# Kernel optimization log

Hardware: AMD Instinct MI355X
Metric: run time of the kernel (lower is better)

The kernel has to match this reference:

```python
import jax, jax.numpy as jnp
import numpy as np

ALLPASS_DELAYS = [225, 556, 441, 341]
ALLPASS_G = 0.7
COMB_DELAYS = [1116, 1188, 1277, 1356]
COMB_FEEDBACKS = [0.84, 0.82, 0.80, 0.78]


def _lagged_first_order(x, N, g, allpass):
    """Fixed-lag first-order recurrence along axis 0, vectorized over axis 1.

    allpass: y[n] = -g*y[n-N] + x[n] + g*x[n-N]  (n >= N), y[n<N] = 0
    comb:    y[n] =  g*y[n-N] + x[n]             (n >= N), y[n<N] = 0

    The recurrence decouples into N independent stride-N subsequences, so we
    reshape to [blocks, N, W] and lax.scan over blocks (T/N steps instead of T).
    """
    T, W = x.shape
    blocks = -(-T // N)
    Tp = blocks * N
    xb = jnp.pad(x, ((0, Tp - T), (0, 0))).reshape(blocks, N, W)
    zero_blk = jnp.zeros((1, N, W), x.dtype)
    if allpass:
        # drive u[k] = x[k] + g*x[k-1]; block 0 output is forced to zero
        u = jnp.concatenate([zero_blk, xb[1:] + g * xb[:-1]], axis=0)
        a = -g
    else:
        # comb: drive u[k] = x[k] for k>=1; block 0 output is zero
        u = jnp.concatenate([zero_blk, xb[1:]], axis=0)
        a = g

    def step(prev, uk):
        y = uk + a * prev
        return y, y

    _, yb = jax.lax.scan(step, jnp.zeros((N, W), x.dtype), u)
    return yb.reshape(Tp, W)[:T]


def setup_inputs() -> dict:
    key = jax.random.key(0)
    T, W = 131072, 128
    x = jax.random.normal(key, (T, W), dtype=jnp.float32)
    return {"x": x}


def reference(x):
    # Series allpass chain
    for N in ALLPASS_DELAYS:
        x = _lagged_first_order(x, N, ALLPASS_G, allpass=True)
    # Parallel feedback comb bank, summed
    comb = jnp.zeros_like(x)
    for N, g in zip(COMB_DELAYS, COMB_FEEDBACKS):
        comb = comb + _lagged_first_order(x, N, g, allpass=False)
    # Original applies eye(T) @ comb and slices [:, :W]; both are identity ops,
    # so we return comb directly (same math, without materializing a TxT eye).
    return comb
```

## Files before the change

kernel.cpp:

```cpp
#include <hip/hip_runtime.h>


constexpr int W = 128;

template <int V> struct fv { float d[V]; };

template <int V>
__device__ __forceinline__ fv<V> fv_zero() {
  fv<V> r;
#pragma unroll
  for (int c = 0; c < V; ++c) r.d[c] = 0.f;
  return r;
}
using fv2 = fv<2>;
using fv4 = fv<4>;

template <int K, bool PRED, int V>
__device__ __forceinline__
void fmarch_blk(const fv<V>* __restrict__ sb, int n0, int N, int laneoff,
                int Tn, float a, fv<V>& yp, fv<V>* __restrict__ y) {
  constexpr int RW = W / V;
  fv<V> xs[K];
#pragma unroll
  for (int u = 0; u < K; ++u) {
    const int n = n0 + u * N;
    xs[u] = (!PRED || n < Tn) ? sb[n * RW + laneoff] : fv_zero<V>();
  }
#pragma unroll
  for (int u = 0; u < K; ++u) {
#pragma unroll
    for (int c = 0; c < V; ++c)
      yp.d[c] = fmaf(a, yp.d[c], xs[u].d[c]);
    y[u] = yp;
  }
}

template <int CNT, bool PRED, int V, int U>
__device__ __forceinline__
void fmarch_seg(const fv<V>* __restrict__ sb, int n0, int N, int laneoff,
                int Tn, float a, fv<V>& yp, fv<V>* __restrict__ y) {
  constexpr int NB = CNT / U, R = CNT % U;
#pragma unroll
  for (int b = 0; b < NB; ++b)
    fmarch_blk<U, PRED, V>(sb, n0 + b * U * N, N, laneoff, Tn, a, yp, y + b * U);
  if constexpr (R > 0)
    fmarch_blk<R, PRED, V>(sb, n0 + NB * U * N, N, laneoff, Tn, a, yp,
                           y + NB * U);
}

template <int MODE, int K, bool PRED, int V>
__device__ __forceinline__
void fstore_blk(fv<V>* __restrict__ out, int n0, int N, int laneoff, int Tn,
                float a, fv<V> Yin, const fv<V>* __restrict__ y, float& p) {
  constexpr int RW = W / V;
  fv<V> os[K];
  if constexpr (MODE == 2) {
#pragma unroll
    for (int u = 0; u < K; ++u) {
      const int n = n0 + u * N;
      os[u] = (!PRED || n < Tn) ? out[n * RW + laneoff] : fv_zero<V>();
    }
  }
#pragma unroll
  for (int u = 0; u < K; ++u) {
    const int n = n0 + u * N;
    fv<V> v;
#pragma unroll
    for (int c = 0; c < V; ++c) {
      v.d[c] = fmaf(p, Yin.d[c], y[u].d[c]);
      if constexpr (MODE == 2) v.d[c] += os[u].d[c];
    }
    if (!PRED || n < Tn) out[n * RW + laneoff] = v;
    p *= a;
  }
}

template <int MODE, int CNT, bool PRED, int V, int U>
__device__ __forceinline__
void fstore_seg(fv<V>* __restrict__ out, int n0, int N, int laneoff, int Tn,
                float a, fv<V> Yin, const fv<V>* __restrict__ y, float p0) {
  constexpr int NB = CNT / U, R = CNT % U;
  float p = p0;
#pragma unroll
  for (int b = 0; b < NB; ++b)
    fstore_blk<MODE, U, PRED, V>(out, n0 + b * U * N, N, laneoff, Tn, a, Yin,
                                 y + b * U, p);
  if constexpr (R > 0)
    fstore_blk<MODE, R, PRED, V>(out, n0 + NB * U * N, N, laneoff, Tn, a, Yin,
                                 y + NB * U, p);
}

template <int MODE, int S, int L, int UM, int US>
__global__ __launch_bounds__(S * 64, 3)
void fcomb(const fv2* __restrict__ sb, fv2* __restrict__ out,
           int N, float g, float aL, int T, int items) {
  const float a = g;
  __shared__ fv2 C[S][64];
  const int tid = threadIdx.x;
  const int s  = tid >> 6;
  const int l6 = tid & 63;

  for (int item = blockIdx.x; item < items; item += gridDim.x) {
    const int r  = item;
    const int n0 = s * L * N + r;

    fv2 y[L];
    fv2 yp = fv_zero<2>();

    if (s == 0) {
      y[0] = fv_zero<2>();
      fmarch_seg<L - 1, false, 2, UM>(sb, n0 + N, N, l6, T, a, yp, y + 1);
    } else if (s < S - 1) {
      fmarch_seg<L, false, 2, UM>(sb, n0, N, l6, T, a, yp, y);
    } else {
      fmarch_seg<L, true, 2, UM>(sb, n0, N, l6, T, a, yp, y);
    }
    C[s][l6] = yp;
    __syncthreads();

    fv2 Yin = fv_zero<2>();
    for (int j = 0; j < s; ++j) {
#pragma unroll
      for (int c = 0; c < 2; ++c)
        Yin.d[c] = fmaf(aL, Yin.d[c], C[j][l6].d[c]);
    }
    __syncthreads();

    if (s < S - 1)
      fstore_seg<MODE, L, false, 2, US>(out, n0, N, l6, T, a, Yin, y, a);
    else
      fstore_seg<MODE, L, true, 2, US>(out, n0, N, l6, T, a, Yin, y, a);
  }
}

__global__ __launch_bounds__(1024)
void prep_s(const fv4* __restrict__ x, fv4* __restrict__ sb) {
  const int e = blockIdx.x * 1024 + threadIdx.x;
  const int n  = e >> 5;
  const int lo = e & 31;
  const int q1 = n / 225, r1 = n - q1 * 225;
  const int q2 = n / 556, r2 = n - q2 * 556;
  const float LG = -0.5145731728297583f;
  const float m1 = exp2f((float)q1 * LG);
  const float m2 = exp2f((float)q2 * LG);
  const float p1 = (q1 & 1) ? -m1 : m1;
  const float p2 = (q2 & 1) ? -m2 : m2;

  const fv4 xs = x[e];
  const fv4 t1 = x[r1 * 32 + lo];
  fv4 t2;
  if (r2 < 225) {
    t2 = fv_zero<4>();
  } else {
    t2 = x[r2 * 32 + lo];
    const int   d = (r2 < 450) ? 225 : 450;
    const float c = (r2 < 450) ? 0.7f : -0.49f;
    const fv4 tt = x[(r2 - d) * 32 + lo];
#pragma unroll
    for (int k = 0; k < 4; ++k) t2.d[k] = fmaf(c, tt.d[k], t2.d[k]);
  }
  fv4 v;
#pragma unroll
  for (int k = 0; k < 4; ++k) {
    float sv = fmaf(-p1, t1.d[k], xs.d[k]);
    v.d[k] = fmaf(-p2, t2.d[k], sv);
  }
  sb[e] = v;
}

constexpr int W2 = 64;
template <int MODE, bool STORE>
__device__ __forceinline__
void g_march(const float2* __restrict__ in, float2* __restrict__ out,
             int n, int N, int cnt, int T, int lane, float g, float a,
             float2& xp, float2& yp) {
  for (int j = 0; j < cnt; ++j) {
    float2 x = (n < T) ? in[n * W2 + lane] : make_float2(0.f, 0.f);
    float ux = (MODE == 0) ? fmaf(g, xp.x, x.x) : x.x;
    float uy = (MODE == 0) ? fmaf(g, xp.y, x.y) : x.y;
    yp.x = fmaf(a, yp.x, ux);
    yp.y = fmaf(a, yp.y, uy);
    xp = x;
    if (STORE && n < T) {
      float2 v = yp;
      if (MODE == 2) { v.x += out[n * W2 + lane].x; v.y += out[n * W2 + lane].y; }
      out[n * W2 + lane] = v;
    }
    n += N;
  }
}

template <int MODE>
__global__ __launch_bounds__(1024)
void stage_gen(const float2* __restrict__ in, float2* __restrict__ out,
               int N, float g, float aL, int L, int T) {
  const float a = (MODE == 0) ? -g : g;
  __shared__ float2 C[16][W2];
  const int tid = threadIdx.x, s = tid >> 6, lane = tid & 63;
  const int r = blockIdx.x;
  if (r >= T) return;
  const int n0 = s * L * N + r;
  if (s == 0) {
    float2 xp = make_float2(0.f, 0.f), yp = make_float2(0.f, 0.f);
    if (MODE == 0) xp = in[r * W2 + lane];
    if (MODE != 2) out[r * W2 + lane] = make_float2(0.f, 0.f);
    g_march<MODE, true>(in, out, r + N, N, L - 1, T, lane, g, a, xp, yp);
    C[0][lane] = yp;
    __syncthreads();
    return;
  }
  {
    float2 xp = make_float2(0.f, 0.f), yp = make_float2(0.f, 0.f);
    if (MODE == 0) xp = in[(n0 - N) * W2 + lane];
    g_march<MODE, false>(in, out, n0, N, L, T, lane, g, a, xp, yp);
    C[s][lane] = yp;
  }
  __syncthreads();
  float2 Yin = make_float2(0.f, 0.f);
  for (int j = 0; j < s; ++j) {
    Yin.x = fmaf(aL, Yin.x, C[j][lane].x);
    Yin.y = fmaf(aL, Yin.y, C[j][lane].y);
  }
  float2 xp = make_float2(0.f, 0.f), yp = Yin;
  if (MODE == 0) xp = in[(n0 - N) * W2 + lane];
  g_march<MODE, true>(in, out, n0, N, L, T, lane, g, a, xp, yp);
}

static void pick_SL(int T, int N, int S0, int* Sp, int* Lp) {
  int Kmin = T / N, Kmax = (T + N - 1) / N;
  int S = S0;
  for (; S > 1; --S) {
    int L = (Kmax + S - 1) / S;
    if ((S - 1) * L <= Kmin) break;
  }
  *Sp = S;
  *Lp = (Kmax + *Sp - 1) / *Sp;
}

static float pow_f(float a, int n) {
  double p = 1.0;
  for (int i = 0; i < n; ++i) p *= (double)a;
  return (float)p;
}

extern "C" void kernel_launch(void* const* d_in, const int* in_sizes, int n_in,
                              void* d_out, int out_size, void* d_ws, size_t ws_size,
                              hipStream_t stream) {
  float* out = (float*)d_out;
  float* ws  = (float*)d_ws;
  const float* x = (const float*)d_in[0];
  const int T = in_sizes[0] / W;

  if (T == 131072) {
    float* sbf = ws;

    hipLaunchKernelGGL(prep_s, dim3(4096), dim3(1024), 0, stream,
                       (const fv4*)x, (fv4*)sbf);

    const fv2* s2 = (const fv2*)sbf;
    fv2* o2 = (fv2*)out;

    hipLaunchKernelGGL((fcomb<1, 8, 15, 4, 4>), dim3(1024), dim3(512),
                       0, stream, s2, o2, 1116, 0.84f, pow_f(0.84f, 15), T, 1116);
    hipLaunchKernelGGL((fcomb<2, 8, 14, 4, 4>), dim3(1024), dim3(512),
                       0, stream, s2, o2, 1188, 0.82f, pow_f(0.82f, 14), T, 1188);
    hipLaunchKernelGGL((fcomb<2, 8, 13, 4, 4>), dim3(1024), dim3(512),
                       0, stream, s2, o2, 1277, 0.80f, pow_f(0.80f, 13), T, 1277);
    hipLaunchKernelGGL((fcomb<2, 8, 13, 4, 4>), dim3(1024), dim3(512),
                       0, stream, s2, o2, 1356, 0.78f, pow_f(0.78f, 13), T, 1356);
  } else {
    const int   apN[4] = {225, 556, 441, 341};
    const int   cbN[4] = {1116, 1188, 1277, 1356};
    const float cbG[4] = {0.84f, 0.82f, 0.80f, 0.78f};
    const float2* src = (const float2*)x;
    float2* bufs[2] = {(float2*)out, (float2*)ws};
    int cur = 0;
    for (int i = 0; i < 4; ++i) {
      int S, L;
      pick_SL(T, apN[i], 16, &S, &L);
      hipLaunchKernelGGL((stage_gen<0>), dim3(apN[i]), dim3(S * 64), 0, stream,
                         src, bufs[cur], apN[i], 0.7f, pow_f(-0.7f, L), L, T);
      src = bufs[cur];
      cur ^= 1;
    }
    float2* dst = (src == (float2*)out) ? (float2*)ws : (float2*)out;
    for (int i = 0; i < 4; ++i) {
      int S, L;
      pick_SL(T, cbN[i], 16, &S, &L);
      if (i == 0)
        hipLaunchKernelGGL((stage_gen<1>), dim3(cbN[i]), dim3(S * 64), 0, stream,
                           src, dst, cbN[i], cbG[i], pow_f(cbG[i], L), L, T);
      else
        hipLaunchKernelGGL((stage_gen<2>), dim3(cbN[i]), dim3(S * 64), 0, stream,
                           src, dst, cbN[i], cbG[i], pow_f(cbG[i], L), L, T);
    }
    if (dst != (float2*)out)
      hipMemcpyAsync(out, dst, (size_t)T * W * sizeof(float),
                     hipMemcpyDeviceToDevice, stream);
  }
}
```

Measured before the change: 227.0 us.

## Fuse allpass prep into first comb pass and store intermediate in fp16

Removes the separate prep_s kernel and computes the allpass-transformed signal inside the first comb kernel, which also writes it out as half precision. The remaining three comb kernels read the fp16 intermediate, halving their input traffic, and unroll their march loads more deeply. The aim is to save one full read-write pass and reduce memory bandwidth. In exchange, precision drops from fp32 to fp16 on the intermediate, which may hurt accuracy. The first kernel also does heavier per-element work, including the gathers at r1 and r2, with lower occupancy (launch bound 2).

```diff
diff --git a/kernel.cpp b/kernel.cpp
--- a/kernel.cpp
+++ b/kernel.cpp
@@ -15,92 +15,157 @@
 using fv2 = fv<2>;
 using fv4 = fv<4>;
 
-template <int K, bool PRED, int V>
-__device__ __forceinline__
-void fmarch_blk(const fv<V>* __restrict__ sb, int n0, int N, int laneoff,
-                int Tn, float a, fv<V>& yp, fv<V>* __restrict__ y) {
-  constexpr int RW = W / V;
-  fv<V> xs[K];
+struct h2 { _Float16 d[2]; };
+
+template <int K, bool PRED>
+__device__ __forceinline__
+void hmarch_blk(const h2* __restrict__ sb, int n0, int N, int lane,
+                int Tn, float a, fv2& yp, fv2* __restrict__ y) {
+  h2 xs[K];
 #pragma unroll
   for (int u = 0; u < K; ++u) {
     const int n = n0 + u * N;
-    xs[u] = (!PRED || n < Tn) ? sb[n * RW + laneoff] : fv_zero<V>();
-  }
-#pragma unroll
-  for (int u = 0; u < K; ++u) {
-#pragma unroll
-    for (int c = 0; c < V; ++c)
-      yp.d[c] = fmaf(a, yp.d[c], xs[u].d[c]);
+    if (!PRED || n < Tn) {
+      xs[u] = sb[n * 64 + lane];
+    } else {
+      xs[u].d[0] = (_Float16)0.f;
+      xs[u].d[1] = (_Float16)0.f;
+    }
+  }
+#pragma unroll
+  for (int u = 0; u < K; ++u) {
+    yp.d[0] = fmaf(a, yp.d[0], (float)xs[u].d[0]);
+    yp.d[1] = fmaf(a, yp.d[1], (float)xs[u].d[1]);
     y[u] = yp;
   }
 }
 
-template <int CNT, bool PRED, int V, int U>
-__device__ __forceinline__
-void fmarch_seg(const fv<V>* __restrict__ sb, int n0, int N, int laneoff,
-                int Tn, float a, fv<V>& yp, fv<V>* __restrict__ y) {
+template <int CNT, bool PRED, int U>
+__device__ __forceinline__
+void hmarch_seg(const h2* __restrict__ sb, int n0, int N, int lane,
+                int Tn, float a, fv2& yp, fv2* __restrict__ y) {
   constexpr int NB = CNT / U, R = CNT % U;
 #pragma unroll
   for (int b = 0; b < NB; ++b)
-    fmarch_blk<U, PRED, V>(sb, n0 + b * U * N, N, laneoff, Tn, a, yp, y + b * U);
+    hmarch_blk<U, PRED>(sb, n0 + b * U * N, N, lane, Tn, a, yp, y + b * U);
   if constexpr (R > 0)
-    fmarch_blk<R, PRED, V>(sb, n0 + NB * U * N, N, laneoff, Tn, a, yp,
-                           y + NB * U);
-}
-
-template <int MODE, int K, bool PRED, int V>
-__device__ __forceinline__
-void fstore_blk(fv<V>* __restrict__ out, int n0, int N, int laneoff, int Tn,
-                float a, fv<V> Yin, const fv<V>* __restrict__ y, float& p) {
-  constexpr int RW = W / V;
-  fv<V> os[K];
+    hmarch_blk<R, PRED>(sb, n0 + NB * U * N, N, lane, Tn, a, yp, y + NB * U);
+}
+
+template <int K, bool PRED>
+__device__ __forceinline__
+void cmarch_blk(const fv2* __restrict__ x, h2* __restrict__ sb,
+                int n0, int N, int lane, int Tn, float a,
+                fv2& yp, fv2* __restrict__ y) {
+  fv2 xs[K], t1[K], t2[K];
+  float p1[K], p2[K];
+#pragma unroll
+  for (int u = 0; u < K; ++u) {
+    const int n = n0 + u * N;
+    const bool ok = !PRED || n < Tn;
+    const int q1 = n / 225, r1 = n - q1 * 225;
+    const int q2 = n / 556, r2 = n - q2 * 556;
+    xs[u] = ok ? x[n * 64 + lane] : fv_zero<2>();
+    t1[u] = x[r1 * 64 + lane];
+    if (r2 < 225) {
+      t2[u] = fv_zero<2>();
+    } else {
+      fv2 b = x[r2 * 64 + lane];
+      const int   d = (r2 < 450) ? 225 : 450;
+      const float c = (r2 < 450) ? 0.7f : -0.49f;
+      fv2 tt = x[(r2 - d) * 64 + lane];
+      t2[u].d[0] = fmaf(c, tt.d[0], b.d[0]);
+      t2[u].d[1] = fmaf(c, tt.d[1], b.d[1]);
+    }
+    const float LG = -0.5145731728297583f;
+    const float m1 = exp2f((float)q1 * LG);
+    const float m2 = exp2f((float)q2 * LG);
+    p1[u] = ok ? ((q1 & 1) ? -m1 : m1) : 0.f;
+    p2[u] = ok ? ((q2 & 1) ? -m2 : m2) : 0.f;
+  }
+#pragma unroll
+  for (int u = 0; u < K; ++u) {
+    const int n = n0 + u * N;
+    fv2 s;
+    s.d[0] = fmaf(-p2[u], t2[u].d[0], fmaf(-p1[u], t1[u].d[0], xs[u].d[0]));
+    s.d[1] = fmaf(-p2[u], t2[u].d[1], fmaf(-p1[u], t1[u].d[1], xs[u].d[1]));
+    if (!PRED || n < Tn) {
+      h2 hh;
+      hh.d[0] = (_Float16)s.d[0];
+      hh.d[1] = (_Float16)s.d[1];
+      sb[n * 64 + lane] = hh;
+    }
+    yp.d[0] = fmaf(a, yp.d[0], s.d[0]);
+    yp.d[1] = fmaf(a, yp.d[1], s.d[1]);
+    y[u] = yp;
+  }
+}
+
+template <int CNT, bool PRED, int U>
+__device__ __forceinline__
+void cmarch_seg(const fv2* __restrict__ x, h2* __restrict__ sb,
+                int n0, int N, int lane, int Tn, float a,
+                fv2& yp, fv2* __restrict__ y) {
+  constexpr int NB = CNT / U, R = CNT % U;
+#pragma unroll
+  for (int b = 0; b < NB; ++b)
+    cmarch_blk<U, PRED>(x, sb, n0 + b * U * N, N, lane, Tn, a, yp, y + b * U);
+  if constexpr (R > 0)
+    cmarch_blk<R, PRED>(x, sb, n0 + NB * U * N, N, lane, Tn, a, yp, y + NB * U);
+}
+
+template <int MODE, int K, bool PRED>
+__device__ __forceinline__
+void fstore_blk(fv2* __restrict__ out, int n0, int N, int lane, int Tn,
+                float a, fv2 Yin, const fv2* __restrict__ y, float& p) {
+  fv2 os[K];
   if constexpr (MODE == 2) {
 #pragma unroll
     for (int u = 0; u < K; ++u) {
       const int n = n0 + u * N;
-      os[u] = (!PRED || n < Tn) ? out[n * RW + laneoff] : fv_zero<V>();
+      os[u] = (!PRED || n < Tn) ? out[n * 64 + lane] : fv_zero<2>();
     }
   }
 #pragma unroll
   for (int u = 0; u < K; ++u) {
     const int n = n0 + u * N;
-    fv<V> v;
-#pragma unroll
-    for (int c = 0; c < V; ++c) {
+    fv2 v;
+#pragma unroll
+    for (int c = 0; c < 2; ++c) {
       v.d[c] = fmaf(p, Yin.d[c], y[u].d[c]);
       if constexpr (MODE == 2) v.d[c] += os[u].d[c];
     }
-    if (!PRED || n < Tn) out[n * RW + laneoff] = v;
+    if (!PRED || n < Tn) out[n * 64 + lane] = v;
     p *= a;
   }
 }
 
-template <int MODE, int CNT, bool PRED, int V, int U>
-__device__ __forceinline__
-void fstore_seg(fv<V>* __restrict__ out, int n0, int N, int laneoff, int Tn,
-                float a, fv<V> Yin, const fv<V>* __restrict__ y, float p0) {
+template <int MODE, int CNT, bool PRED, int U>
+__device__ __forceinline__
+void fstore_seg(fv2* __restrict__ out, int n0, int N, int lane, int Tn,
+                float a, fv2 Yin, const fv2* __restrict__ y, float p0) {
   constexpr int NB = CNT / U, R = CNT % U;
   float p = p0;
 #pragma unroll
   for (int b = 0; b < NB; ++b)
-    fstore_blk<MODE, U, PRED, V>(out, n0 + b * U * N, N, laneoff, Tn, a, Yin,
-                                 y + b * U, p);
+    fstore_blk<MODE, U, PRED>(out, n0 + b * U * N, N, lane, Tn, a, Yin,
+                              y + b * U, p);
   if constexpr (R > 0)
-    fstore_blk<MODE, R, PRED, V>(out, n0 + NB * U * N, N, laneoff, Tn, a, Yin,
-                                 y + NB * U, p);
-}
-
-template <int MODE, int S, int L, int UM, int US>
-__global__ __launch_bounds__(S * 64, 3)
-void fcomb(const fv2* __restrict__ sb, fv2* __restrict__ out,
-           int N, float g, float aL, int T, int items) {
+    fstore_blk<MODE, R, PRED>(out, n0 + NB * U * N, N, lane, Tn, a, Yin,
+                              y + NB * U, p);
+}
+
+template <int S, int L, int UM, int US>
+__global__ __launch_bounds__(S * 64, 2)
+void fcomb1(const fv2* __restrict__ x, h2* __restrict__ sb,
+            fv2* __restrict__ out, int N, float g, float aL, int T) {
   const float a = g;
   __shared__ fv2 C[S][64];
   const int tid = threadIdx.x;
   const int s  = tid >> 6;
   const int l6 = tid & 63;
 
-  for (int item = blockIdx.x; item < items; item += gridDim.x) {
+  for (int item = blockIdx.x; item < N; item += gridDim.x) {
     const int r  = item;
     const int n0 = s * L * N + r;
 
@@ -109,11 +174,11 @@
 
     if (s == 0) {
       y[0] = fv_zero<2>();
-      fmarch_seg<L - 1, false, 2, UM>(sb, n0 + N, N, l6, T, a, yp, y + 1);
+      cmarch_seg<L - 1, false, UM>(x, sb, n0 + N, N, l6, T, a, yp, y + 1);
     } else if (s < S - 1) {
-      fmarch_seg<L, false, 2, UM>(sb, n0, N, l6, T, a, yp, y);
+      cmarch_seg<L, false, UM>(x, sb, n0, N, l6, T, a, yp, y);
     } else {
-      fmarch_seg<L, true, 2, UM>(sb, n0, N, l6, T, a, yp, y);
+      cmarch_seg<L, true, UM>(x, sb, n0, N, l6, T, a, yp, y);
     }
     C[s][l6] = yp;
     __syncthreads();
@@ -127,45 +192,53 @@
     __syncthreads();
 
     if (s < S - 1)
-      fstore_seg<MODE, L, false, 2, US>(out, n0, N, l6, T, a, Yin, y, a);
+      fstore_seg<1, L, false, US>(out, n0, N, l6, T, a, Yin, y, a);
     else
-      fstore_seg<MODE, L, true, 2, US>(out, n0, N, l6, T, a, Yin, y, a);
-  }
-}
-
-__global__ __launch_bounds__(1024)
-void prep_s(const fv4* __restrict__ x, fv4* __restrict__ sb) {
-  const int e = blockIdx.x * 1024 + threadIdx.x;
-  const int n  = e >> 5;
-  const int lo = e & 31;
-  const int q1 = n / 225, r1 = n - q1 * 225;
-  const int q2 = n / 556, r2 = n - q2 * 556;
-  const float LG = -0.5145731728297583f;
-  const float m1 = exp2f((float)q1 * LG);
-  const float m2 = exp2f((float)q2 * LG);
-  const float p1 = (q1 & 1) ? -m1 : m1;
-  const float p2 = (q2 & 1) ? -m2 : m2;
-
-  const fv4 xs = x[e];
-  const fv4 t1 = x[r1 * 32 + lo];
-  fv4 t2;
-  if (r2 < 225) {
-    t2 = fv_zero<4>();
-  } else {
-    t2 = x[r2 * 32 + lo];
-    const int   d = (r2 < 450) ? 225 : 450;
-    const float c = (r2 < 450) ? 0.7f : -0.49f;
-    const fv4 tt = x[(r2 - d) * 32 + lo];
-#pragma unroll
-    for (int k = 0; k < 4; ++k) t2.d[k] = fmaf(c, tt.d[k], t2.d[k]);
-  }
-  fv4 v;
-#pragma unroll
-  for (int k = 0; k < 4; ++k) {
-    float sv = fmaf(-p1, t1.d[k], xs.d[k]);
-    v.d[k] = fmaf(-p2, t2.d[k], sv);
-  }
-  sb[e] = v;
+      fstore_seg<1, L, true, US>(out, n0, N, l6, T, a, Yin, y, a);
+  }
+}
+
+template <int S, int L, int UM, int US>
+__global__ __launch_bounds__(S * 64, 3)
+void fcombh(const h2* __restrict__ sb, fv2* __restrict__ out,
+            int N, float g, float aL, int T) {
+  const float a = g;
+  __shared__ fv2 C[S][64];
+  const int tid = threadIdx.x;
+  const int s  = tid >> 6;
+  const int l6 = tid & 63;
+
+  for (int item = blockIdx.x; item < N; item += gridDim.x) {
+    const int r  = item;
+    const int n0 = s * L * N + r;
+
+    fv2 y[L];
+    fv2 yp = fv_zero<2>();
+
+    if (s == 0) {
+      y[0] = fv_zero<2>();
+      hmarch_seg<L - 1, false, UM>(sb, n0 + N, N, l6, T, a, yp, y + 1);
+    } else if (s < S - 1) {
+      hmarch_seg<L, false, UM>(sb, n0, N, l6, T, a, yp, y);
+    } else {
+      hmarch_seg<L, true, UM>(sb, n0, N, l6, T, a, yp, y);
+    }
+    C[s][l6] = yp;
+    __syncthreads();
+
+    fv2 Yin = fv_zero<2>();
+    for (int j = 0; j < s; ++j) {
+#pragma unroll
+      for (int c = 0; c < 2; ++c)
+        Yin.d[c] = fmaf(aL, Yin.d[c], C[j][l6].d[c]);
+    }
+    __syncthreads();
+
+    if (s < S - 1)
+      fstore_seg<2, L, false, US>(out, n0, N, l6, T, a, Yin, y, a);
+    else
+      fstore_seg<2, L, true, US>(out, n0, N, l6, T, a, Yin, y, a);
+  }
 }
 
 constexpr int W2 = 64;
@@ -252,22 +325,23 @@
   const int T = in_sizes[0] / W;
 
   if (T == 131072) {
-    float* sbf = ws;
-
-    hipLaunchKernelGGL(prep_s, dim3(4096), dim3(1024), 0, stream,
-                       (const fv4*)x, (fv4*)sbf);
-
-    const fv2* s2 = (const fv2*)sbf;
+    h2* sb16 = (h2*)ws;
+
+    const fv2* x2 = (const fv2*)x;
     fv2* o2 = (fv2*)out;
 
-    hipLaunchKernelGGL((fcomb<1, 8, 15, 4, 4>), dim3(1024), dim3(512),
-                       0, stream, s2, o2, 1116, 0.84f, pow_f(0.84f, 15), T, 1116);
-    hipLaunchKernelGGL((fcomb<2, 8, 14, 4, 4>), dim3(1024), dim3(512),
-                       0, stream, s2, o2, 1188, 0.82f, pow_f(0.82f, 14), T, 1188);
-    hipLaunchKernelGGL((fcomb<2, 8, 13, 4, 4>), dim3(1024), dim3(512),
-                       0, stream, s2, o2, 1277, 0.80f, pow_f(0.80f, 13), T, 1277);
-    hipLaunchKernelGGL((fcomb<2, 8, 13, 4, 4>), dim3(1024), dim3(512),
-                       0, stream, s2, o2, 1356, 0.78f, pow_f(0.78f, 13), T, 1356);
+    hipLaunchKernelGGL((fcomb1<8, 15, 2, 4>), dim3(1024), dim3(512),
+                       0, stream, x2, sb16, o2, 1116, 0.84f,
+                       pow_f(0.84f, 15), T);
+    hipLaunchKernelGGL((fcombh<8, 14, 8, 4>), dim3(1024), dim3(512),
+                       0, stream, (const h2*)sb16, o2, 1188, 0.82f,
+                       pow_f(0.82f, 14), T);
+    hipLaunchKernelGGL((fcombh<8, 13, 8, 4>), dim3(1024), dim3(512),
+                       0, stream, (const h2*)sb16, o2, 1277, 0.80f,
+                       pow_f(0.80f, 13), T);
+    hipLaunchKernelGGL((fcombh<8, 13, 8, 4>), dim3(1024), dim3(512),
+                       0, stream, (const h2*)sb16, o2, 1356, 0.78f,
+                       pow_f(0.78f, 13), T);
   } else {
     const int   apN[4] = {225, 556, 441, 341};
     const int   cbN[4] = {1116, 1188, 1277, 1356};
```

New measurement: 239.0 us. +5.3%, slower.
